# Optimization experiments

Measured on AMD Instinct MI355X. Metric: run time of the kernel, lower is better.

Reference implementation:

```python
import jax, jax.numpy as jnp
import numpy as np

N, E, F, H = 100000, 1000000, 128, 64
BN_EPS = 1e-3  # keras BatchNormalization default epsilon


def setup_inputs() -> dict:
    key = jax.random.key(0)
    k_x, k_src, k_dst, k_w = jax.random.split(key, 4)
    node_features = jax.random.normal(k_x, (N, F), dtype=jnp.float32)
    # Ensure every node appears at least once as a source so that
    # deg**-0.5 is finite (the original code implicitly assumes this).
    src = jnp.concatenate([
        jnp.arange(N, dtype=jnp.int32),
        jax.random.randint(k_src, (E - N,), 0, N, dtype=jnp.int32),
    ])
    dst = jax.random.randint(k_dst, (E,), 0, N, dtype=jnp.int32)
    edge_index = jnp.stack([src, dst], axis=1)  # [E, 2]
    # glorot_uniform for kernel
    limit = np.sqrt(6.0 / (F + H)).astype(np.float32)
    W = jax.random.uniform(k_w, (F, H), dtype=jnp.float32, minval=-limit, maxval=limit)
    b = jnp.zeros((H,), dtype=jnp.float32)
    bn_gamma = jnp.ones((H,), dtype=jnp.float32)
    bn_beta = jnp.zeros((H,), dtype=jnp.float32)
    bn_mean = jnp.zeros((H,), dtype=jnp.float32)
    bn_var = jnp.ones((H,), dtype=jnp.float32)
    return dict(node_features=node_features, W=W, b=b, bn_gamma=bn_gamma,
                bn_beta=bn_beta, bn_mean=bn_mean, bn_var=bn_var,
                edge_index=edge_index)


def reference(node_features, W, b, bn_gamma, bn_beta, bn_mean, bn_var, edge_index):
    n = node_features.shape[0]
    src = edge_index[:, 0]
    dst = edge_index[:, 1]
    # Dense transform; dropout is identity in inference (training=False).
    h = node_features @ W + b  # [N, H]
    # Out-degree per node (segments keyed by src, matching the TF code).
    deg = jax.ops.segment_sum(jnp.ones(src.shape, h.dtype), src, num_segments=n)  # [N]
    inv_sqrt_deg = deg ** -0.5
    # Per-edge symmetric-style scaling: deg(src)^-0.5 * deg(dst)^-0.5 * h[dst]
    edge_scale = inv_sqrt_deg[src] * inv_sqrt_deg[dst]  # [E]
    neigh = edge_scale[:, None] * h[dst]  # [E, H]
    agg = 0.5 * jax.ops.segment_sum(neigh, src, num_segments=n)  # [N, H]
    # Self term: segment_mean of deg(src) * h[src] over src segments.
    self_term = deg[src][:, None] * h[src]  # [E, H]
    self_sum = jax.ops.segment_sum(self_term, src, num_segments=n)  # [N, H]
    self_mean = self_sum / jnp.maximum(deg, 1.0)[:, None]
    agg = agg + 0.5 * self_mean
    # BatchNormalization in inference mode.
    out = (agg - bn_mean) * (bn_gamma * jax.lax.rsqrt(bn_var + BN_EPS)) + bn_beta
    return out
```

## Files before the change

### kernel.cpp

```cpp
#include <hip/hip_runtime.h>

#define BN_EPS 0.001f
#define CAP 32
#define NPART 8
#define SEGE 4096
#define ABLK 8

typedef __attribute__((ext_vector_type(8))) short bf16x8;
typedef __attribute__((ext_vector_type(4))) float f32x4;

__device__ __forceinline__ unsigned short f2bf(float f) {
  unsigned u = __float_as_uint(f);
  u += 0x7fffu + ((u >> 16) & 1u);
  return (unsigned short)(u >> 16);
}
__device__ __forceinline__ float bfLO(unsigned u) { return __uint_as_float(u << 16); }
__device__ __forceinline__ float bfHI(unsigned u) { return __uint_as_float(u & 0xffff0000u); }

__global__ __launch_bounds__(256) void k_fused(
    const float* __restrict__ X, const float* __restrict__ W,
    const float* __restrict__ B, unsigned short* __restrict__ hb, int N, int Gg,
    const int2* __restrict__ ei, int* __restrict__ cnt,
    int* __restrict__ ell_t, int E) {
  __shared__ float WtF[4096];

  int bid = blockIdx.x;
  int tid = threadIdx.x;
  int gid = bid >> 4;
  int slot = bid & 15;

  if (slot < 8) {
    int p = slot;
    int lo = (int)((long long)p * N / NPART);
    int hi = (int)((long long)(p + 1) * N / NPART);
    const int4* e4 = (const int4*)ei;
    int n4 = E >> 1;
    int base4 = gid * (SEGE / 2);
    #pragma unroll
    for (int i = 0; i < 8; ++i) {
      int q = base4 + i * 256 + tid;
      if (q < n4) {
        int4 v = e4[q];
        if (v.x >= lo && v.x < hi) {
          int pos = atomicAdd(&cnt[v.x], 1);
          if (pos < CAP) ell_t[(size_t)pos * N + v.x] = v.y;
        }
        if (v.z >= lo && v.z < hi) {
          int pos = atomicAdd(&cnt[v.z], 1);
          if (pos < CAP) ell_t[(size_t)pos * N + v.z] = v.w;
        }
      }
    }
    if ((E & 1) && gid == 0 && tid == 0) {
      int2 sd = ei[E - 1];
      if (sd.x >= lo && sd.x < hi) {
        int pos = atomicAdd(&cnt[sd.x], 1);
        if (pos < CAP) ell_t[(size_t)pos * N + sd.x] = sd.y;
      }
    }
    return;
  }

  int tile = gid * 8 + (slot - 8);
  if (tile >= Gg) return;

  char* Wt = (char*)WtF;
  const float4* W4 = (const float4*)W;
  for (int i = tid; i < 2048; i += 256) {
    float4 v = W4[i];
    int k = i >> 4;
    int col0 = (i & 15) << 2;
    int kb2 = k << 1;
    *(unsigned short*)(Wt + (((col0 + 0) << 8) | (kb2 ^ (((col0 + 0) & 7) << 4)))) = f2bf(v.x);
    *(unsigned short*)(Wt + (((col0 + 1) << 8) | (kb2 ^ (((col0 + 1) & 7) << 4)))) = f2bf(v.y);
    *(unsigned short*)(Wt + (((col0 + 2) << 8) | (kb2 ^ (((col0 + 2) & 7) << 4)))) = f2bf(v.z);
    *(unsigned short*)(Wt + (((col0 + 3) << 8) | (kb2 ^ (((col0 + 3) & 7) << 4)))) = f2bf(v.w);
  }
  __syncthreads();

  int lane = tid & 63;
  int w = tid >> 6;
  int l15 = lane & 15;
  int lk = lane >> 4;

  int row0 = tile * 64;
  int rA = row0 + w * 16 + l15;
  bool rowok = rA < N;
  const float* xp = X + (size_t)rA * 128 + (lk << 3);

  f32x4 acc[4];
  #pragma unroll
  for (int n = 0; n < 4; ++n) {
    float bv = B[(n << 4) + l15];
    acc[n] = (f32x4){bv, bv, bv, bv};
  }

  #pragma unroll
  for (int kb = 0; kb < 4; ++kb) {
    bf16x8 af = {0, 0, 0, 0, 0, 0, 0, 0};
    if (rowok) {
      float4 x0 = *(const float4*)(xp + kb * 32);
      float4 x1 = *(const float4*)(xp + kb * 32 + 4);
      af[0] = (short)f2bf(x0.x); af[1] = (short)f2bf(x0.y);
      af[2] = (short)f2bf(x0.z); af[3] = (short)f2bf(x0.w);
      af[4] = (short)f2bf(x1.x); af[5] = (short)f2bf(x1.y);
      af[6] = (short)f2bf(x1.z); af[7] = (short)f2bf(x1.w);
    }
    int kbyte = (kb << 6) | (lk << 4);
    #pragma unroll
    for (int n = 0; n < 4; ++n) {
      int col = (n << 4) + l15;
      bf16x8 bfr = *(const bf16x8*)(Wt + ((col << 8) | (kbyte ^ ((col & 7) << 4))));
      acc[n] = __builtin_amdgcn_mfma_f32_16x16x32_bf16(af, bfr, acc[n], 0, 0, 0);
    }
  }

  int rbase = row0 + w * 16 + (lk << 2);
  #pragma unroll
  for (int n = 0; n < 4; ++n) {
    #pragma unroll
    for (int q = 0; q < 4; ++q) {
      int row = rbase + q;
      if (row < N) hb[(size_t)row * 64 + (n << 4) + l15] = f2bf(acc[n][q]);
    }
  }
}

__global__ __launch_bounds__(256) void k_agg(const int* __restrict__ cnt,
                                             const int* __restrict__ ell_t,
                                             const uint2* __restrict__ hb64,
                                             const float* __restrict__ gamma,
                                             const float* __restrict__ beta,
                                             const float* __restrict__ mean,
                                             const float* __restrict__ var,
                                             float* __restrict__ out, int N) {
  __shared__ int lds_dst[CAP * ABLK];

  int tid = threadIdx.x;
  int node0 = blockIdx.x * ABLK;

  {
    int j = tid & (ABLK - 1);
    int p = tid >> 3;
    int n = node0 + j;
    lds_dst[p * ABLK + j] = (n < N) ? ell_t[(size_t)p * N + n] : 0;
  }

  int hw = tid >> 5;
  int lane32 = tid & 31;
  int sl = lane32 & 15;
  int hf = lane32 >> 4;
  int node = node0 + hw;

  float4 gm = *(const float4*)&gamma[sl * 4];
  float4 bt = *(const float4*)&beta[sl * 4];
  float4 mn = *(const float4*)&mean[sl * 4];
  float4 vr = *(const float4*)&var[sl * 4];
  float gs0 = gm.x * rsqrtf(vr.x + BN_EPS);
  float gs1 = gm.y * rsqrtf(vr.y + BN_EPS);
  float gs2 = gm.z * rsqrtf(vr.z + BN_EPS);
  float gs3 = gm.w * rsqrtf(vr.w + BN_EPS);

  __syncthreads();
  if (node >= N) return;

  int c0 = cnt[node];
  int c = (c0 < CAP) ? c0 : CAP;
  uint2 us = hb64[(size_t)node * 16 + sl];

  float a0 = 0.f, a1 = 0.f, a2 = 0.f, a3 = 0.f;
  int npair = (c + 1) >> 1;
  int pq = 0;
  for (; pq + 4 <= npair; pq += 4) {
    int d[4]; float vmask[4];
    #pragma unroll
    for (int i = 0; i < 4; ++i) {
      int e = 2 * (pq + i) + hf;
      bool vld = e < c;
      int dr = vld ? lds_dst[e * ABLK + hw] : 0;
      d[i] = ((unsigned)dr < (unsigned)N) ? dr : 0;
      vmask[i] = vld ? 1.f : 0.f;
    }
    int cc[4];
    #pragma unroll
    for (int i = 0; i < 4; ++i) cc[i] = cnt[d[i]];
    uint2 u[4];
    #pragma unroll
    for (int i = 0; i < 4; ++i) u[i] = hb64[(size_t)d[i] * 16 + sl];
    #pragma unroll
    for (int i = 0; i < 4; ++i) {
      float s = vmask[i] * rsqrtf((float)((cc[i] > 0) ? cc[i] : 1));
      a0 = fmaf(s, bfLO(u[i].x), a0);
      a1 = fmaf(s, bfHI(u[i].x), a1);
      a2 = fmaf(s, bfLO(u[i].y), a2);
      a3 = fmaf(s, bfHI(u[i].y), a3);
    }
  }
  for (; pq < npair; ++pq) {
    int e = 2 * pq + hf;
    bool vld = e < c;
    int dr = vld ? lds_dst[e * ABLK + hw] : 0;
    int d = ((unsigned)dr < (unsigned)N) ? dr : 0;
    int cq = cnt[d];
    uint2 u = hb64[(size_t)d * 16 + sl];
    float s = (vld ? 1.f : 0.f) * rsqrtf((float)((cq > 0) ? cq : 1));
    a0 = fmaf(s, bfLO(u.x), a0);
    a1 = fmaf(s, bfHI(u.x), a1);
    a2 = fmaf(s, bfLO(u.y), a2);
    a3 = fmaf(s, bfHI(u.y), a3);
  }

  a0 += __shfl_xor(a0, 16);
  a1 += __shfl_xor(a1, 16);
  a2 += __shfl_xor(a2, 16);
  a3 += __shfl_xor(a3, 16);

  float degf = (float)c0;
  float isd = rsqrtf((float)((c0 > 0) ? c0 : 1));
  float r0 = 0.5f * (isd * a0 + degf * bfLO(us.x));
  float r1 = 0.5f * (isd * a1 + degf * bfHI(us.x));
  float r2 = 0.5f * (isd * a2 + degf * bfLO(us.y));
  float r3 = 0.5f * (isd * a3 + degf * bfHI(us.y));

  if (hf == 0) {
    float4 o;
    o.x = (r0 - mn.x) * gs0 + bt.x;
    o.y = (r1 - mn.y) * gs1 + bt.y;
    o.z = (r2 - mn.z) * gs2 + bt.z;
    o.w = (r3 - mn.w) * gs3 + bt.w;
    *(float4*)&out[(size_t)node * 64 + sl * 4] = o;
  }
}

extern "C" void kernel_launch(void* const* d_in, const int* in_sizes, int n_in,
                              void* d_out, int out_size, void* d_ws, size_t ws_size,
                              hipStream_t stream) {
  const float* X     = (const float*)d_in[0];
  const float* W     = (const float*)d_in[1];
  const float* B     = (const float*)d_in[2];
  const float* gamma = (const float*)d_in[3];
  const float* beta  = (const float*)d_in[4];
  const float* mean  = (const float*)d_in[5];
  const float* var   = (const float*)d_in[6];
  const int2*  ei    = (const int2*)d_in[7];

  int N = in_sizes[0] / 128;
  int E = in_sizes[7] / 2;
  float* out = (float*)d_out;

  unsigned short* hb  = (unsigned short*)d_ws;
  int*            ell = (int*)(hb + (size_t)N * 64);
  int*            cnt = ell + (size_t)N * CAP;

  (void)hipMemsetAsync(cnt, 0, (size_t)N * sizeof(int), stream);

  int Gg = (N + 63) / 64;
  int nsegs = (E + SEGE - 1) / SEGE;
  int ngg = (Gg + 7) / 8;
  int ngroups = (nsegs > ngg) ? nsegs : ngg;
  k_fused<<<ngroups * 16, 256, 0, stream>>>(X, W, B, hb, N, Gg, ei, cnt, ell, E);

  int Ga = (N + ABLK - 1) / ABLK;
  k_agg<<<Ga, 256, 0, stream>>>(cnt, ell, (const uint2*)hb,
                                gamma, beta, mean, var, out, N);
}
```

Before: 171.4 us.

## Schedule GEMM blocks before edge scatter, widen aggregation gathers to 16 bytes

The fused kernel's grid is reordered so all GEMM tiles come first, followed by the ELL-building scatter blocks. The scatter blocks spin with a bounded sleep on a global flag that GEMM blocks increment, so the GEMM work is scheduled ahead of the atomics-heavy scatter. The aggregation kernel now has each lane load 8 bf16 values (uint4) with 4 edges in flight per node instead of 2, and it folds the batchnorm mean into a precomputed bias. The risks are idle spin-waiting in the scatter blocks and more shuffle reductions.

```diff
diff --git a/kernel.cpp b/kernel.cpp
--- a/kernel.cpp
+++ b/kernel.cpp
@@ -21,21 +21,30 @@
     const float* __restrict__ X, const float* __restrict__ W,
     const float* __restrict__ B, unsigned short* __restrict__ hb, int N, int Gg,
     const int2* __restrict__ ei, int* __restrict__ cnt,
-    int* __restrict__ ell_t, int E) {
+    int* __restrict__ ell_t, int E, int gemmPad, int* __restrict__ flag) {
   __shared__ float WtF[4096];
 
   int bid = blockIdx.x;
   int tid = threadIdx.x;
-  int gid = bid >> 4;
-  int slot = bid & 15;
-
-  if (slot < 8) {
-    int p = slot;
+
+  if (bid >= gemmPad) {
+    int p = bid & 7;
+    int seg = (bid - gemmPad) >> 3;
+    if (tid == 0) {
+      int spins = 0;
+      while (__hip_atomic_load(flag, __ATOMIC_RELAXED, __HIP_MEMORY_SCOPE_AGENT) < Gg
+             && spins < 192) {
+        __builtin_amdgcn_s_sleep(8);
+        ++spins;
+      }
+    }
+    __syncthreads();
+
     int lo = (int)((long long)p * N / NPART);
     int hi = (int)((long long)(p + 1) * N / NPART);
     const int4* e4 = (const int4*)ei;
     int n4 = E >> 1;
-    int base4 = gid * (SEGE / 2);
+    int base4 = seg * (SEGE / 2);
     #pragma unroll
     for (int i = 0; i < 8; ++i) {
       int q = base4 + i * 256 + tid;
@@ -51,7 +60,7 @@
         }
       }
     }
-    if ((E & 1) && gid == 0 && tid == 0) {
+    if ((E & 1) && seg == 0 && tid == 0) {
       int2 sd = ei[E - 1];
       if (sd.x >= lo && sd.x < hi) {
         int pos = atomicAdd(&cnt[sd.x], 1);
@@ -61,8 +70,9 @@
     return;
   }
 
-  int tile = gid * 8 + (slot - 8);
-  if (tile >= Gg) return;
+  if (bid >= Gg) return;
+
+  int tile = bid;
 
   char* Wt = (char*)WtF;
   const float4* W4 = (const float4*)W;
@@ -124,11 +134,19 @@
       if (row < N) hb[(size_t)row * 64 + (n << 4) + l15] = f2bf(acc[n][q]);
     }
   }
-}
+  __syncthreads();
+  if (tid == 0) atomicAdd(flag, 1);
+}
+
+#define ACC8(u, s)                                            \
+  a0 = fmaf(s, bfLO(u.x), a0); a1 = fmaf(s, bfHI(u.x), a1);   \
+  a2 = fmaf(s, bfLO(u.y), a2); a3 = fmaf(s, bfHI(u.y), a3);   \
+  a4 = fmaf(s, bfLO(u.z), a4); a5 = fmaf(s, bfHI(u.z), a5);   \
+  a6 = fmaf(s, bfLO(u.w), a6); a7 = fmaf(s, bfHI(u.w), a7);
 
 __global__ __launch_bounds__(256) void k_agg(const int* __restrict__ cnt,
                                              const int* __restrict__ ell_t,
-                                             const uint2* __restrict__ hb64,
+                                             const uint4* __restrict__ hb128,
                                              const float* __restrict__ gamma,
                                              const float* __restrict__ beta,
                                              const float* __restrict__ mean,
@@ -148,87 +166,92 @@
 
   int hw = tid >> 5;
   int lane32 = tid & 31;
-  int sl = lane32 & 15;
-  int hf = lane32 >> 4;
+  int sl = lane32 & 7;
+  int eg = lane32 >> 3;
   int node = node0 + hw;
 
-  float4 gm = *(const float4*)&gamma[sl * 4];
-  float4 bt = *(const float4*)&beta[sl * 4];
-  float4 mn = *(const float4*)&mean[sl * 4];
-  float4 vr = *(const float4*)&var[sl * 4];
-  float gs0 = gm.x * rsqrtf(vr.x + BN_EPS);
-  float gs1 = gm.y * rsqrtf(vr.y + BN_EPS);
-  float gs2 = gm.z * rsqrtf(vr.z + BN_EPS);
-  float gs3 = gm.w * rsqrtf(vr.w + BN_EPS);
+  float4 gA = *(const float4*)&gamma[sl * 8];
+  float4 gB = *(const float4*)&gamma[sl * 8 + 4];
+  float4 bA = *(const float4*)&beta[sl * 8];
+  float4 bB = *(const float4*)&beta[sl * 8 + 4];
+  float4 mA = *(const float4*)&mean[sl * 8];
+  float4 mB = *(const float4*)&mean[sl * 8 + 4];
+  float4 vA = *(const float4*)&var[sl * 8];
+  float4 vB = *(const float4*)&var[sl * 8 + 4];
+  float gs0 = gA.x * rsqrtf(vA.x + BN_EPS), bp0 = bA.x - mA.x * gs0;
+  float gs1 = gA.y * rsqrtf(vA.y + BN_EPS), bp1 = bA.y - mA.y * gs1;
+  float gs2 = gA.z * rsqrtf(vA.z + BN_EPS), bp2 = bA.z - mA.z * gs2;
+  float gs3 = gA.w * rsqrtf(vA.w + BN_EPS), bp3 = bA.w - mA.w * gs3;
+  float gs4 = gB.x * rsqrtf(vB.x + BN_EPS), bp4 = bB.x - mB.x * gs4;
+  float gs5 = gB.y * rsqrtf(vB.y + BN_EPS), bp5 = bB.y - mB.y * gs5;
+  float gs6 = gB.z * rsqrtf(vB.z + BN_EPS), bp6 = bB.z - mB.z * gs6;
+  float gs7 = gB.w * rsqrtf(vB.w + BN_EPS), bp7 = bB.w - mB.w * gs7;
 
   __syncthreads();
   if (node >= N) return;
 
   int c0 = cnt[node];
   int c = (c0 < CAP) ? c0 : CAP;
-  uint2 us = hb64[(size_t)node * 16 + sl];
+  uint4 us = hb128[(size_t)node * 8 + sl];
 
   float a0 = 0.f, a1 = 0.f, a2 = 0.f, a3 = 0.f;
-  int npair = (c + 1) >> 1;
-  int pq = 0;
-  for (; pq + 4 <= npair; pq += 4) {
-    int d[4]; float vmask[4];
-    #pragma unroll
-    for (int i = 0; i < 4; ++i) {
-      int e = 2 * (pq + i) + hf;
-      bool vld = e < c;
-      int dr = vld ? lds_dst[e * ABLK + hw] : 0;
-      d[i] = ((unsigned)dr < (unsigned)N) ? dr : 0;
-      vmask[i] = vld ? 1.f : 0.f;
-    }
-    int cc[4];
-    #pragma unroll
-    for (int i = 0; i < 4; ++i) cc[i] = cnt[d[i]];
-    uint2 u[4];
-    #pragma unroll
-    for (int i = 0; i < 4; ++i) u[i] = hb64[(size_t)d[i] * 16 + sl];
-    #pragma unroll
-    for (int i = 0; i < 4; ++i) {
-      float s = vmask[i] * rsqrtf((float)((cc[i] > 0) ? cc[i] : 1));
-      a0 = fmaf(s, bfLO(u[i].x), a0);
-      a1 = fmaf(s, bfHI(u[i].x), a1);
-      a2 = fmaf(s, bfLO(u[i].y), a2);
-      a3 = fmaf(s, bfHI(u[i].y), a3);
-    }
-  }
-  for (; pq < npair; ++pq) {
-    int e = 2 * pq + hf;
-    bool vld = e < c;
-    int dr = vld ? lds_dst[e * ABLK + hw] : 0;
+  float a4 = 0.f, a5 = 0.f, a6 = 0.f, a7 = 0.f;
+
+  int nst = (c + 3) >> 2;
+  int st = 0;
+  for (; st + 2 <= nst; st += 2) {
+    int e0 = 4 * st + eg, e1 = 4 * (st + 1) + eg;
+    int dr0 = (e0 < c) ? lds_dst[e0 * ABLK + hw] : 0;
+    int dr1 = (e1 < c) ? lds_dst[e1 * ABLK + hw] : 0;
+    float v0 = (e0 < c) ? 1.f : 0.f;
+    float v1 = (e1 < c) ? 1.f : 0.f;
+    int d0 = ((unsigned)dr0 < (unsigned)N) ? dr0 : 0;
+    int d1 = ((unsigned)dr1 < (unsigned)N) ? dr1 : 0;
+    int c0_ = cnt[d0], c1_ = cnt[d1];
+    uint4 u0 = hb128[(size_t)d0 * 8 + sl];
+    uint4 u1 = hb128[(size_t)d1 * 8 + sl];
+    float s0 = v0 * rsqrtf((float)((c0_ > 0) ? c0_ : 1));
+    float s1 = v1 * rsqrtf((float)((c1_ > 0) ? c1_ : 1));
+    ACC8(u0, s0);
+    ACC8(u1, s1);
+  }
+  for (; st < nst; ++st) {
+    int e = 4 * st + eg;
+    int dr = (e < c) ? lds_dst[e * ABLK + hw] : 0;
+    float v = (e < c) ? 1.f : 0.f;
     int d = ((unsigned)dr < (unsigned)N) ? dr : 0;
     int cq = cnt[d];
-    uint2 u = hb64[(size_t)d * 16 + sl];
-    float s = (vld ? 1.f : 0.f) * rsqrtf((float)((cq > 0) ? cq : 1));
-    a0 = fmaf(s, bfLO(u.x), a0);
-    a1 = fmaf(s, bfHI(u.x), a1);
-    a2 = fmaf(s, bfLO(u.y), a2);
-    a3 = fmaf(s, bfHI(u.y), a3);
-  }
-
-  a0 += __shfl_xor(a0, 16);
-  a1 += __shfl_xor(a1, 16);
-  a2 += __shfl_xor(a2, 16);
-  a3 += __shfl_xor(a3, 16);
-
-  float degf = (float)c0;
-  float isd = rsqrtf((float)((c0 > 0) ? c0 : 1));
-  float r0 = 0.5f * (isd * a0 + degf * bfLO(us.x));
-  float r1 = 0.5f * (isd * a1 + degf * bfHI(us.x));
-  float r2 = 0.5f * (isd * a2 + degf * bfLO(us.y));
-  float r3 = 0.5f * (isd * a3 + degf * bfHI(us.y));
-
-  if (hf == 0) {
-    float4 o;
-    o.x = (r0 - mn.x) * gs0 + bt.x;
-    o.y = (r1 - mn.y) * gs1 + bt.y;
-    o.z = (r2 - mn.z) * gs2 + bt.z;
-    o.w = (r3 - mn.w) * gs3 + bt.w;
-    *(float4*)&out[(size_t)node * 64 + sl * 4] = o;
+    uint4 u = hb128[(size_t)d * 8 + sl];
+    float s = v * rsqrtf((float)((cq > 0) ? cq : 1));
+    ACC8(u, s);
+  }
+
+  a0 += __shfl_xor(a0, 8);  a0 += __shfl_xor(a0, 16);
+  a1 += __shfl_xor(a1, 8);  a1 += __shfl_xor(a1, 16);
+  a2 += __shfl_xor(a2, 8);  a2 += __shfl_xor(a2, 16);
+  a3 += __shfl_xor(a3, 8);  a3 += __shfl_xor(a3, 16);
+  a4 += __shfl_xor(a4, 8);  a4 += __shfl_xor(a4, 16);
+  a5 += __shfl_xor(a5, 8);  a5 += __shfl_xor(a5, 16);
+  a6 += __shfl_xor(a6, 8);  a6 += __shfl_xor(a6, 16);
+  a7 += __shfl_xor(a7, 8);  a7 += __shfl_xor(a7, 16);
+
+  if (eg == 0) {
+    float degf = (float)c0;
+    float isd = rsqrtf((float)((c0 > 0) ? c0 : 1));
+    float r0 = 0.5f * (isd * a0 + degf * bfLO(us.x));
+    float r1 = 0.5f * (isd * a1 + degf * bfHI(us.x));
+    float r2 = 0.5f * (isd * a2 + degf * bfLO(us.y));
+    float r3 = 0.5f * (isd * a3 + degf * bfHI(us.y));
+    float r4 = 0.5f * (isd * a4 + degf * bfLO(us.z));
+    float r5 = 0.5f * (isd * a5 + degf * bfHI(us.z));
+    float r6 = 0.5f * (isd * a6 + degf * bfLO(us.w));
+    float r7 = 0.5f * (isd * a7 + degf * bfHI(us.w));
+    float4 oA = make_float4(r0 * gs0 + bp0, r1 * gs1 + bp1,
+                            r2 * gs2 + bp2, r3 * gs3 + bp3);
+    float4 oB = make_float4(r4 * gs4 + bp4, r5 * gs5 + bp5,
+                            r6 * gs6 + bp6, r7 * gs7 + bp7);
+    *(float4*)&out[(size_t)node * 64 + sl * 8] = oA;
+    *(float4*)&out[(size_t)node * 64 + sl * 8 + 4] = oB;
   }
 }
 
@@ -248,19 +271,20 @@
   int E = in_sizes[7] / 2;
   float* out = (float*)d_out;
 
-  unsigned short* hb  = (unsigned short*)d_ws;
-  int*            ell = (int*)(hb + (size_t)N * 64);
-  int*            cnt = ell + (size_t)N * CAP;
-
-  (void)hipMemsetAsync(cnt, 0, (size_t)N * sizeof(int), stream);
+  unsigned short* hb   = (unsigned short*)d_ws;
+  int*            ell  = (int*)(hb + (size_t)N * 64);
+  int*            cnt  = ell + (size_t)N * CAP;
+  int*            flag = cnt + N;
+
+  (void)hipMemsetAsync(cnt, 0, ((size_t)N + 1) * sizeof(int), stream);
 
   int Gg = (N + 63) / 64;
+  int gemmPad = (Gg + 7) & ~7;
   int nsegs = (E + SEGE - 1) / SEGE;
-  int ngg = (Gg + 7) / 8;
-  int ngroups = (nsegs > ngg) ? nsegs : ngg;
-  k_fused<<<ngroups * 16, 256, 0, stream>>>(X, W, B, hb, N, Gg, ei, cnt, ell, E);
+  int grid = gemmPad + nsegs * 8;
+  k_fused<<<grid, 256, 0, stream>>>(X, W, B, hb, N, Gg, ei, cnt, ell, E, gemmPad, flag);
 
   int Ga = (N + ABLK - 1) / ABLK;
-  k_agg<<<Ga, 256, 0, stream>>>(cnt, ell, (const uint2*)hb,
+  k_agg<<<Ga, 256, 0, stream>>>(cnt, ell, (const uint4*)hb,
                                 gamma, beta, mean, var, out, N);
 }
```

Result: slower. 316.8 us (+84.9%).
